# Kernel tuning notes

Hardware: AMD Instinct MI355X
Metric: run time of the kernel (lower is better)

## Reference

```python
import jax, jax.numpy as jnp
import numpy as np

B, C, H, W = 32, 256, 56, 56
G, K, RR = 4, 7, 4
CR = C // RR


def setup_inputs() -> dict:
    key = jax.random.key(0)
    ks = jax.random.split(key, 10)
    s = jax.random.normal(ks[0], (B, C, H, W), jnp.float32)
    r = jax.random.normal(ks[1], (B, C, H, W), jnp.float32)
    b1 = 1.0 / np.sqrt(C)
    proj_w1 = jax.random.uniform(ks[2], (CR, C), jnp.float32, -b1, b1)
    proj_b1 = jax.random.uniform(ks[3], (CR,), jnp.float32, -b1, b1)
    b2 = 1.0 / np.sqrt(CR)
    proj_w2 = jax.random.uniform(ks[4], (C * G * 2, CR), jnp.float32, -b2, b2)
    proj_b2 = jax.random.uniform(ks[5], (C * G * 2,), jnp.float32, -b2, b2)
    # kaiming_uniform_(a=sqrt(5)) on [G, C, K, K]: fan_in = C*K*K, bound = sqrt(6/((1+5)*fan_in)) = 1/sqrt(fan_in)
    bw = 1.0 / np.sqrt(C * K * K)
    weight = jax.random.uniform(ks[6], (G, C, K, K), jnp.float32, -bw, bw)
    beta_scale = jnp.zeros((G, C), jnp.float32)  # original is [1,G,C,1,1] zeros
    bp = 1.0 / np.sqrt(C)
    pw_w = jax.random.uniform(ks[7], (C, C), jnp.float32, -bp, bp)
    pw_b = jax.random.uniform(ks[8], (C,), jnp.float32, -bp, bp)
    return {"s": s, "r": r, "proj_w1": proj_w1, "proj_b1": proj_b1,
            "proj_w2": proj_w2, "proj_b2": proj_b2, "weight": weight,
            "beta_scale": beta_scale, "pw_w": pw_w, "pw_b": pw_b}


def reference(s, r, proj_w1, proj_b1, proj_w2, proj_b2, weight, beta_scale, pw_w, pw_b):
    Bs, Cs, Hs, Ws = s.shape
    Gs, _, Ks, _ = weight.shape
    # squeeze-excite weight generation
    pooled = jnp.mean(r, axis=(2, 3))                                   # [B,C]
    h = jax.nn.gelu(pooled @ proj_w1.T + proj_b1, approximate=False)    # [B,C//rr]
    scale = (h @ proj_w2.T + proj_b2).reshape(Bs, Gs, Cs, 2)            # [B,G,C,2]
    alpha = jax.nn.softmax(scale[..., 0], axis=1)                       # softmax over groups
    beta = jnp.tanh(scale[..., 1] * jnp.exp(beta_scale)[None] * 0.1)    # [B,G,C]
    w = alpha[..., None, None] * weight[None] + beta[..., None, None]   # [B,G,C,K,K]
    # sum over groups == summing per-group depthwise conv outputs (conv linear in kernel)
    wk = jnp.sum(w, axis=1).reshape(Bs * Cs, 1, Ks, Ks)
    pad = Ks // 2
    out = jax.lax.conv_general_dilated(
        s.reshape(1, Bs * Cs, Hs, Ws), wk,
        window_strides=(1, 1), padding=[(pad, pad), (pad, pad)],
        dimension_numbers=("NCHW", "OIHW", "NCHW"),
        feature_group_count=Bs * Cs)                                     # [1,B*C,H,W]
    out = jax.nn.gelu(out, approximate=False).reshape(Bs, Cs, Hs, Ws)
    out = jnp.einsum("bchw,dc->bdhw", out, pw_w) + pw_b[None, :, None, None]
    return out
```

## Files before the change

kernel.cpp:

```cpp
#include <hip/hip_runtime.h>
#include <math.h>

typedef unsigned short u16;
typedef unsigned int   u32;
typedef __attribute__((ext_vector_type(8))) short  short8;
typedef __attribute__((ext_vector_type(4))) float  floatx4;

#define Bn  32
#define Cn  256
#define HWn 3136
#define Gn  4
#define CRn 64

__device__ __forceinline__ float gelu_f(float x) {
    return 0.5f * x * (1.0f + erff(x * 0.70710678118654752f));
}
__device__ __forceinline__ float gelu_fast(float x) {
    float ax = fabsf(x);
    float y  = ax * 0.70710678118654752f;
    float t  = __builtin_amdgcn_rcpf(fmaf(0.3275911f, y, 1.0f));
    float p  = fmaf(fmaf(fmaf(fmaf(1.061405429f, t, -1.453152027f), t,
                              1.421413741f), t, -0.284496736f), t, 0.254829592f) * t;
    float e  = __builtin_amdgcn_exp2f(-y * y * 1.442695040888963f);
    float er = fmaf(-p, e, 1.0f);
    return fmaf(0.5f * ax, er, 0.5f * x);
}
__device__ __forceinline__ u16 f2bf(float f) {
    u32 u = __builtin_bit_cast(u32, f);
    u = (u + 0x7fffu + ((u >> 16) & 1u)) >> 16;
    return (u16)u;
}

__global__ __launch_bounds__(256) void k_pool(const float* __restrict__ r,
                                              const float* __restrict__ pw_w,
                                              float* __restrict__ pooled,
                                              u16* __restrict__ wbf) {
    int blk = blockIdx.x, t = threadIdx.x;
    if (blk >= Bn * Cn) {
        int base = (blk - Bn * Cn) * 1024 + t;
        #pragma unroll
        for (int i = 0; i < 4; i++) wbf[base + i * 256] = f2bf(pw_w[base + i * 256]);
        return;
    }
    const float4* src = (const float4*)(r + (size_t)blk * HWn);
    float sum = 0.f;
    for (int i = t; i < HWn / 4; i += 256) {
        float4 v = src[i];
        sum += (v.x + v.y) + (v.z + v.w);
    }
    #pragma unroll
    for (int off = 32; off >= 1; off >>= 1) sum += __shfl_down(sum, off, 64);
    __shared__ float red[4];
    if ((t & 63) == 0) red[t >> 6] = sum;
    __syncthreads();
    if (t == 0) pooled[blk] = (red[0] + red[1] + red[2] + red[3]) * (1.0f / 3136.0f);
}

__global__ __launch_bounds__(256) void k_wgen(const float* __restrict__ pooled,
                                              const float* __restrict__ w1,
                                              const float* __restrict__ b1,
                                              const float* __restrict__ w2,
                                              const float* __restrict__ b2,
                                              const float* __restrict__ weight,
                                              const float* __restrict__ beta_scale,
                                              float* __restrict__ wk) {
    int b = blockIdx.x, t = threadIdx.x;
    __shared__ float sp[Cn];
    __shared__ float sh[CRn];
    __shared__ float ssc[Cn * Gn * 2];
    sp[t] = pooled[b * Cn + t];
    __syncthreads();
    if (t < CRn) {
        float acc = b1[t];
        const float* wr = w1 + t * Cn;
        for (int c = 0; c < Cn; c++) acc += sp[c] * wr[c];
        sh[t] = gelu_f(acc);
    }
    __syncthreads();
    for (int i = t; i < Cn * Gn * 2; i += 256) {
        float acc = b2[i];
        const float* wr = w2 + i * CRn;
        #pragma unroll 8
        for (int j = 0; j < CRn; j++) acc += sh[j] * wr[j];
        ssc[i] = acc;
    }
    __syncthreads();
    float av[Gn], bt[Gn];
    float mx = -1e30f;
    #pragma unroll
    for (int g = 0; g < Gn; g++) {
        av[g] = ssc[(g * Cn + t) * 2 + 0];
        float s1 = ssc[(g * Cn + t) * 2 + 1];
        bt[g] = tanhf(s1 * expf(beta_scale[g * Cn + t]) * 0.1f);
        mx = fmaxf(mx, av[g]);
    }
    float se = 0.f;
    #pragma unroll
    for (int g = 0; g < Gn; g++) { av[g] = expf(av[g] - mx); se += av[g]; }
    float inv = 1.0f / se;
    #pragma unroll
    for (int g = 0; g < Gn; g++) av[g] *= inv;
    float bsum = bt[0] + bt[1] + bt[2] + bt[3];
    float* out = wk + ((size_t)b * Cn + t) * 49;
    for (int kk = 0; kk < 49; kk++) {
        float w = bsum;
        #pragma unroll
        for (int g = 0; g < Gn; g++) w += av[g] * weight[(g * Cn + t) * 49 + kk];
        out[kk] = w;
    }
}

__global__ __launch_bounds__(128) void k_dw(const float* __restrict__ s,
                                            const float* __restrict__ wk,
                                            u16* __restrict__ xdw) {
    int bc = blockIdx.x, t = threadIdx.x;
    __shared__ float kw[49];
    __shared__ float sin_[62 * 62];
    {
        float4 z = {0.f, 0.f, 0.f, 0.f};
        float4* p = (float4*)sin_;
        for (int i = t; i < 961; i += 128) p[i] = z;
    }
    if (t < 49) kw[t] = wk[(size_t)bc * 49 + t];
    __syncthreads();
    const float4* src = (const float4*)(s + (size_t)bc * HWn);
    for (int i = t; i < HWn / 4; i += 128) {
        float4 v = src[i];
        int row = i / 14;
        int col = (i % 14) * 4;
        float* dst = &sin_[(row + 3) * 62 + col + 3];
        dst[0] = v.x; dst[1] = v.y; dst[2] = v.z; dst[3] = v.w;
    }
    __syncthreads();
    if (t < 112) {
        int r0 = (t / 14) * 7, c0 = (t % 14) * 4;
        float acc[7][4] = {};
        #pragma unroll
        for (int a = 0; a < 13; a++) {
            float row10[10];
            const float* rp = &sin_[(r0 + a) * 62 + c0];
            #pragma unroll
            for (int x = 0; x < 10; x++) row10[x] = rp[x];
            #pragma unroll
            for (int i = 0; i < 7; i++) {
                int ky = a - i;
                if (ky >= 0 && ky < 7) {
                    #pragma unroll
                    for (int kx = 0; kx < 7; kx++) {
                        float wv = kw[ky * 7 + kx];
                        #pragma unroll
                        for (int j = 0; j < 4; j++) acc[i][j] += row10[j + kx] * wv;
                    }
                }
            }
        }
        u16* dst = xdw + (size_t)bc * HWn;
        #pragma unroll
        for (int i = 0; i < 7; i++) {
            u16 ov[4];
            #pragma unroll
            for (int j = 0; j < 4; j++) ov[j] = f2bf(gelu_fast(acc[i][j]));
            *(uint2*)(dst + (r0 + i) * 56 + c0) = *(const uint2*)ov;
        }
    }
}

__global__ __launch_bounds__(256) void k_pw(const u16* __restrict__ xdw,
                                            const u16* __restrict__ wbf,
                                            const float* __restrict__ pw_b,
                                            float* __restrict__ out) {
    int tileHW = blockIdx.x;
    int b      = blockIdx.y;
    int t = threadIdx.x;
    int lane = t & 63;
    int wv = t >> 6;
    int hw0 = tileHW * 64;

    __shared__ __align__(16) u16 sA[256 * 40];
    __shared__ __align__(16) u16 sX[64 * 40];

    floatx4 acc[4][4];
    #pragma unroll
    for (int mi = 0; mi < 4; mi++)
        #pragma unroll
        for (int ni = 0; ni < 4; ni++) acc[mi][ni] = (floatx4){0.f, 0.f, 0.f, 0.f};

    int arow = t >> 2;
    int akc  = t & 3;
    int xc   = t >> 3;
    int xhc  = t & 7;
    int wgrp = (xc >> 3) ^ (xhc & 3);
    int scol = (wgrp << 3) | (xc & 7);

    const u16* Xbase = xdw + (size_t)b * Cn * HWn;
    int q = lane >> 4, l16 = lane & 15;

    for (int ks = 0; ks < 8; ks++) {
        int k0 = ks * 32;
        __syncthreads();
        #pragma unroll
        for (int quarter = 0; quarter < 4; quarter++) {
            int dd = arow + quarter * 64;
            short8 v = *(const short8*)(wbf + dd * 256 + k0 + akc * 8);
            *(short8*)(&sA[dd * 40 + akc * 8]) = v;
        }
        {
            short8 v = *(const short8*)(Xbase + (size_t)(k0 + xc) * HWn + hw0 + xhc * 8);
            const u16* vp = (const u16*)&v;
            #pragma unroll
            for (int e = 0; e < 8; e++) sX[(xhc * 8 + e) * 40 + scol] = vp[e];
        }
        __syncthreads();
        short8 fa[4], fb[4];
        #pragma unroll
        for (int mi = 0; mi < 4; mi++) {
            int row = wv * 64 + mi * 16 + l16;
            fa[mi] = *(const short8*)(&sA[row * 40 + q * 8]);
        }
        #pragma unroll
        for (int ni = 0; ni < 4; ni++) {
            int hwRow = ni * 16 + l16;
            int rgrp = q ^ ((hwRow >> 3) & 3);
            fb[ni] = *(const short8*)(&sX[hwRow * 40 + rgrp * 8]);
        }
        #pragma unroll
        for (int mi = 0; mi < 4; mi++)
            #pragma unroll
            for (int ni = 0; ni < 4; ni++)
                acc[mi][ni] = __builtin_amdgcn_mfma_f32_16x16x32_bf16(fa[mi], fb[ni], acc[mi][ni], 0, 0, 0);
    }
    #pragma unroll
    for (int mi = 0; mi < 4; mi++) {
        #pragma unroll
        for (int reg = 0; reg < 4; reg++) {
            int d = wv * 64 + mi * 16 + q * 4 + reg;
            float bias = pw_b[d];
            #pragma unroll
            for (int ni = 0; ni < 4; ni++) {
                int hw = hw0 + ni * 16 + l16;
                out[((size_t)b * Cn + d) * HWn + hw] = acc[mi][ni][reg] + bias;
            }
        }
    }
}

extern "C" void kernel_launch(void* const* d_in, const int* in_sizes, int n_in,
                              void* d_out, int out_size, void* d_ws, size_t ws_size,
                              hipStream_t stream) {
    const float* s          = (const float*)d_in[0];
    const float* r          = (const float*)d_in[1];
    const float* proj_w1    = (const float*)d_in[2];
    const float* proj_b1    = (const float*)d_in[3];
    const float* proj_w2    = (const float*)d_in[4];
    const float* proj_b2    = (const float*)d_in[5];
    const float* weight     = (const float*)d_in[6];
    const float* beta_scale = (const float*)d_in[7];
    const float* pw_w       = (const float*)d_in[8];
    const float* pw_b       = (const float*)d_in[9];
    float* out = (float*)d_out;

    char* ws = (char*)d_ws;
    float* pooled = (float*)(ws);
    u16*   wbf    = (u16*)(ws + 32768);
    float* wk     = (float*)(ws + 163840);
    u16*   xdw    = (u16*)(ws + 2097152);

    k_pool<<<Bn * Cn + 64, 256, 0, stream>>>(r, pw_w, pooled, wbf);
    k_wgen<<<Bn, 256, 0, stream>>>(pooled, proj_w1, proj_b1, proj_w2, proj_b2,
                                   weight, beta_scale, wk);
    k_dw<<<Bn * Cn, 128, 0, stream>>>(s, wk, xdw);
    k_pw<<<dim3(49, Bn), 256, 0, stream>>>(xdw, wbf, pw_b, out);
}
```

Measured before the change: 365.4 us.

## Restructure depthwise conv to one wavefront per channel with 7x7 register tiles

The depthwise conv kernel now maps one 64-lane wavefront to each (batch, channel) plane, with four planes per 256-thread block. Each lane computes a 7x7 output tile instead of 7x4, and the kernel weights are held in registers. This removes the block-level barriers, the 16 idle threads per block and the shared-memory weight loads, and improves input reuse per loaded row. In exchange it uses many more registers per lane, a larger padded LDS footprint, and scalar 2-byte output stores instead of 8-byte vector stores.

```diff
diff --git a/kernel.cpp b/kernel.cpp
--- a/kernel.cpp
+++ b/kernel.cpp
@@ -110,58 +110,62 @@
     }
 }
 
-__global__ __launch_bounds__(128) void k_dw(const float* __restrict__ s,
-                                            const float* __restrict__ wk,
-                                            u16* __restrict__ xdw) {
-    int bc = blockIdx.x, t = threadIdx.x;
-    __shared__ float kw[49];
-    __shared__ float sin_[62 * 62];
+#define DW_S 68
+__global__ __launch_bounds__(256, 2) void k_dw(const float* __restrict__ s,
+                                               const float* __restrict__ wk,
+                                               u16* __restrict__ xdw) {
+    int t = threadIdx.x;
+    int wv = __builtin_amdgcn_readfirstlane(t >> 6);
+    int lane = t & 63;
+    int bc = blockIdx.x * 4 + wv;
+
+    __shared__ float sbuf[4][62 * DW_S];
+    float* buf = sbuf[wv];
+
     {
         float4 z = {0.f, 0.f, 0.f, 0.f};
-        float4* p = (float4*)sin_;
-        for (int i = t; i < 961; i += 128) p[i] = z;
-    }
-    if (t < 49) kw[t] = wk[(size_t)bc * 49 + t];
-    __syncthreads();
+        float4* p = (float4*)buf;
+        for (int i = lane; i < (62 * DW_S) / 4; i += 64) p[i] = z;
+    }
     const float4* src = (const float4*)(s + (size_t)bc * HWn);
-    for (int i = t; i < HWn / 4; i += 128) {
+    for (int i = lane; i < 784; i += 64) {
         float4 v = src[i];
-        int row = i / 14;
-        int col = (i % 14) * 4;
-        float* dst = &sin_[(row + 3) * 62 + col + 3];
-        dst[0] = v.x; dst[1] = v.y; dst[2] = v.z; dst[3] = v.w;
-    }
-    __syncthreads();
-    if (t < 112) {
-        int r0 = (t / 14) * 7, c0 = (t % 14) * 4;
-        float acc[7][4] = {};
-        #pragma unroll
-        for (int a = 0; a < 13; a++) {
-            float row10[10];
-            const float* rp = &sin_[(r0 + a) * 62 + c0];
-            #pragma unroll
-            for (int x = 0; x < 10; x++) row10[x] = rp[x];
-            #pragma unroll
-            for (int i = 0; i < 7; i++) {
-                int ky = a - i;
-                if (ky >= 0 && ky < 7) {
+        int row = i / 14, col = (i % 14) * 4;
+        *(float4*)&buf[(row + 3) * DW_S + 4 + col] = v;
+    }
+    const float* kwp = wk + (size_t)bc * 49;
+    float kw[49];
+    #pragma unroll
+    for (int k = 0; k < 49; k++) kw[k] = kwp[k];
+
+    int r0 = (lane >> 3) * 7, c0 = (lane & 7) * 7;
+    float acc[7][7] = {};
+    #pragma unroll
+    for (int a = 0; a < 13; a++) {
+        float rv[13];
+        const float* rp = &buf[(r0 + a) * DW_S + c0 + 1];
+        #pragma unroll
+        for (int x = 0; x < 13; x++) rv[x] = rp[x];
+        #pragma unroll
+        for (int i = 0; i < 7; i++) {
+            int ky = a - i;
+            if (ky >= 0 && ky < 7) {
+                #pragma unroll
+                for (int kx = 0; kx < 7; kx++) {
+                    float w = kw[ky * 7 + kx];
                     #pragma unroll
-                    for (int kx = 0; kx < 7; kx++) {
-                        float wv = kw[ky * 7 + kx];
-                        #pragma unroll
-                        for (int j = 0; j < 4; j++) acc[i][j] += row10[j + kx] * wv;
-                    }
+                    for (int j = 0; j < 7; j++)
+                        acc[i][j] = fmaf(rv[j + kx], w, acc[i][j]);
                 }
             }
         }
-        u16* dst = xdw + (size_t)bc * HWn;
-        #pragma unroll
-        for (int i = 0; i < 7; i++) {
-            u16 ov[4];
-            #pragma unroll
-            for (int j = 0; j < 4; j++) ov[j] = f2bf(gelu_fast(acc[i][j]));
-            *(uint2*)(dst + (r0 + i) * 56 + c0) = *(const uint2*)ov;
-        }
+    }
+    u16* dst = xdw + (size_t)bc * HWn;
+    #pragma unroll
+    for (int i = 0; i < 7; i++) {
+        #pragma unroll
+        for (int j = 0; j < 7; j++)
+            dst[(r0 + i) * 56 + c0 + j] = f2bf(gelu_fast(acc[i][j]));
     }
 }
 
@@ -268,6 +272,6 @@
     k_pool<<<Bn * Cn + 64, 256, 0, stream>>>(r, pw_w, pooled, wbf);
     k_wgen<<<Bn, 256, 0, stream>>>(pooled, proj_w1, proj_b1, proj_w2, proj_b2,
                                    weight, beta_scale, wk);
-    k_dw<<<Bn * Cn, 128, 0, stream>>>(s, wk, xdw);
+    k_dw<<<(Bn * Cn) / 4, 256, 0, stream>>>(s, wk, xdw);
     k_pw<<<dim3(49, Bn), 256, 0, stream>>>(xdw, wbf, pw_b, out);
 }
```

After: 378.3 us. 3.5% more time.
